# Performance work log

Hardware: AMD Instinct MI355X
Metric: run time of the kernel (lower is better)

Reference implementation:

```python
import jax, jax.numpy as jnp
import numpy as np

PAD = 0
B, M, N, E = 32, 512, 512, 768
NEG_INF = 1e12
SCALE = np.float32(np.sqrt(768.0))


def submult(a, b):
    d = a - b
    return jnp.concatenate([a, b, d, a * b, d * d], axis=-1)


def setup_inputs() -> dict:
    key = jax.random.key(0)
    ks = jax.random.split(key, 8)
    c_ids = jax.random.randint(ks[0], (B, M), 1, 30000)
    c_ids = c_ids.at[:, 3 * M // 4 :].set(PAD)  # trailing padding
    r_ids = jax.random.randint(ks[1], (B, N), 1, 30000)
    r_ids = r_ids.at[:, 3 * N // 4 :].set(PAD)
    c_hs = jax.random.normal(ks[2], (B, M, E), dtype=jnp.float32)
    r_hs = jax.random.normal(ks[3], (B, N, E), dtype=jnp.float32)
    W_pre = jax.random.normal(ks[4], (5 * E, E), dtype=jnp.float32) * 0.02
    b_pre = jnp.zeros((E,), dtype=jnp.float32)
    W_ff1 = jax.random.normal(ks[5], (15 * E, E), dtype=jnp.float32) * 0.02
    b_ff1 = jnp.zeros((E,), dtype=jnp.float32)
    W_ff2 = jax.random.normal(ks[6], (E, 1), dtype=jnp.float32) * 0.02
    b_ff2 = jnp.zeros((1,), dtype=jnp.float32)
    return {
        "c_ids": c_ids, "r_ids": r_ids, "c_hs": c_hs, "r_hs": r_hs,
        "W_pre": W_pre, "b_pre": b_pre,
        "W_ff1": W_ff1, "b_ff1": b_ff1, "W_ff2": W_ff2, "b_ff2": b_ff2,
    }


def reference(c_ids, r_ids, c_hs, r_hs, W_pre, b_pre, W_ff1, b_ff1, W_ff2, b_ff2):
    cm = c_ids != PAD  # [B,M]
    rm = r_ids != PAD  # [B,N]
    # bidirectional cross-attention
    att = jnp.einsum("bme,bne->bmn", c_hs, r_hs) / SCALE
    pair_mask = cm[:, :, None] & rm[:, None, :]
    att = jnp.where(pair_mask, att, -NEG_INF)
    c_hat = jnp.einsum("bne,bmn->bme", r_hs, jax.nn.softmax(att, axis=-1))
    r_hat = jnp.einsum("bme,bmn->bne", c_hs, jax.nn.softmax(att, axis=-2))
    # submult expansion + pre_rnn (Linear + ReLU)
    c_bar = jax.nn.relu(submult(c_hat, c_hs) @ W_pre + b_pre)  # [B,M,E]
    r_bar = jax.nn.relu(submult(r_hat, r_hs) @ W_pre + b_pre)  # [B,N,E]
    # zero out padded positions
    c_x = jnp.where(cm[:, :, None], c_bar, 0.0)
    r_x = jnp.where(rm[:, :, None], r_bar, 0.0)
    c_cnt = cm.sum(-1).astype(c_x.dtype)[:, None]
    r_cnt = rm.sum(-1).astype(r_x.dtype)[:, None]
    c_feat = jnp.concatenate([c_x[:, 0], c_x.sum(1) / c_cnt, c_x.max(1)], axis=-1)
    r_feat = jnp.concatenate([r_x[:, 0], r_x.sum(1) / r_cnt, r_x.max(1)], axis=-1)
    m_vs = submult(c_feat, r_feat)  # [B, 15*E]
    h = jax.nn.relu(m_vs @ W_ff1 + b_ff1)
    scores = (h @ W_ff2 + b_ff2)[:, 0]  # [B]
    return scores
```

## Files before the change

### kernel.cpp

```cpp
#include <hip/hip_runtime.h>
#include <math.h>

#define B_ 32
#define M_ 512
#define N_ 512
#define E_ 768
#define NEG_BIG   -1e12f
#define INV_SCALE 0.03608439182435161f

typedef __attribute__((ext_vector_type(8))) __bf16 bf16x8;
typedef __attribute__((ext_vector_type(4))) float  floatx4;

#define MFMA_BF16 __builtin_amdgcn_mfma_f32_16x16x32_bf16

#define BAR() do { asm volatile("s_waitcnt lgkmcnt(0)" ::: "memory"); \
                   __builtin_amdgcn_s_barrier(); } while (0)

__device__ __forceinline__ void load16(const float* __restrict__ p, float* v) {
    *(float4*)&v[0]  = *(const float4*)(p);
    *(float4*)&v[4]  = *(const float4*)(p + 4);
    *(float4*)&v[8]  = *(const float4*)(p + 8);
    *(float4*)&v[12] = *(const float4*)(p + 12);
}

__device__ __forceinline__ void cvt_store16(const float* v, __bf16* hi, __bf16* lo,
                                            int row, int h) {
    bf16x8 h0, h1, l0, l1;
#pragma unroll
    for (int j = 0; j < 8; ++j) {
        float x0 = v[j], x1 = v[j + 8];
        __bf16 a0 = (__bf16)x0;
        __bf16 a1 = (__bf16)x1;
        h0[j] = a0;
        h1[j] = a1;
        l0[j] = (__bf16)(x0 - (float)a0);
        l1[j] = (__bf16)(x1 - (float)a1);
    }
    const int xr = (row >> 1) & 3;
    *(bf16x8*)&hi[row * 32 + (((2 * h)     ^ xr) << 3)] = h0;
    *(bf16x8*)&hi[row * 32 + (((2 * h + 1) ^ xr) << 3)] = h1;
    *(bf16x8*)&lo[row * 32 + (((2 * h)     ^ xr) << 3)] = l0;
    *(bf16x8*)&lo[row * 32 + (((2 * h + 1) ^ xr) << 3)] = l1;
}

__device__ __forceinline__ void store_pre16(const bf16x8* v, __bf16* hi, __bf16* lo,
                                            int row, int h) {
    const int xr = (row >> 1) & 3;
    *(bf16x8*)&hi[row * 32 + (((2 * h)     ^ xr) << 3)] = v[0];
    *(bf16x8*)&hi[row * 32 + (((2 * h + 1) ^ xr) << 3)] = v[1];
    *(bf16x8*)&lo[row * 32 + (((2 * h)     ^ xr) << 3)] = v[2];
    *(bf16x8*)&lo[row * 32 + (((2 * h + 1) ^ xr) << 3)] = v[3];
}

__device__ __forceinline__ void mfma_step(const __bf16* Ahi, const __bf16* Alo,
                                          const __bf16* Bhi, const __bf16* Blo,
                                          const int (&aoff)[4], const int (&boff)[4],
                                          floatx4 (&acc)[4][4]) {
    bf16x8 bh[4], bl[4];
#pragma unroll
    for (int fn = 0; fn < 4; ++fn) {
        bh[fn] = *(const bf16x8*)&Bhi[boff[fn]];
        bl[fn] = *(const bf16x8*)&Blo[boff[fn]];
    }
#pragma unroll
    for (int fm = 0; fm < 4; ++fm) {
        bf16x8 ah = *(const bf16x8*)&Ahi[aoff[fm]];
        bf16x8 al = *(const bf16x8*)&Alo[aoff[fm]];
#pragma unroll
        for (int fn = 0; fn < 4; ++fn) {
            acc[fm][fn] = MFMA_BF16(ah, bh[fn], acc[fm][fn], 0, 0, 0);
            acc[fm][fn] = MFMA_BF16(ah, bl[fn], acc[fm][fn], 0, 0, 0);
            acc[fm][fn] = MFMA_BF16(al, bh[fn], acc[fm][fn], 0, 0, 0);
        }
    }
}

#define TILE_SETUP()                                                      \
    const int tid = threadIdx.x, lane = tid & 63;                         \
    const int l15 = lane & 15, l4 = lane >> 4;                            \
    const int wid = tid >> 6, wm = wid >> 1, wn = wid & 1;                \
    const int srow = tid >> 1, h = tid & 1;                               \
    int aoff[4], boff[4];                                                 \
    _Pragma("unroll")                                                     \
    for (int f = 0; f < 4; ++f) {                                         \
        int rr = wm * 64 + f * 16 + l15;                                  \
        aoff[f] = rr * 32 + ((l4 ^ ((rr >> 1) & 3)) << 3);                \
        int cc = wn * 64 + f * 16 + l15;                                  \
        boff[f] = cc * 32 + ((l4 ^ ((cc >> 1) & 3)) << 3);                \
    }                                                                     \
    floatx4 acc[4][4];                                                    \
    const floatx4 zero_ = {0.f, 0.f, 0.f, 0.f};                           \
    _Pragma("unroll")                                                     \
    for (int i = 0; i < 4; ++i)                                           \
        _Pragma("unroll")                                                 \
        for (int j = 0; j < 4; ++j) acc[i][j] = zero_;

__global__ __launch_bounds__(256, 2)
void mfma_att(const float* __restrict__ chs, const float* __restrict__ rhs,
              const int* __restrict__ cids, const int* __restrict__ rids,
              float* __restrict__ att) {
    __shared__ __bf16 Ahi[4096], Alo[4096], Bhi[4096], Blo[4096];
    const int b = blockIdx.z, m0 = blockIdx.x * 128, n0 = blockIdx.y * 128;
    TILE_SETUP();
    const float* Ap = chs + ((size_t)b * M_ + m0 + srow) * E_ + h * 16;
    const float* Bp = rhs + ((size_t)b * N_ + n0 + srow) * E_ + h * 16;

    float va[16], vb[16], na[16], nb[16];
    load16(Ap, va); load16(Bp, vb);
#pragma unroll 1
    for (int k0 = 0; k0 < E_; k0 += 64) {
        BAR();
        cvt_store16(va, Ahi, Alo, srow, h);
        cvt_store16(vb, Bhi, Blo, srow, h);
        load16(Ap + k0 + 32, na);
        load16(Bp + k0 + 32, nb);
        BAR();
        mfma_step(Ahi, Alo, Bhi, Blo, aoff, boff, acc);
        BAR();
        cvt_store16(na, Ahi, Alo, srow, h);
        cvt_store16(nb, Bhi, Blo, srow, h);
        if (k0 + 64 < E_) { load16(Ap + k0 + 64, va); load16(Bp + k0 + 64, vb); }
        BAR();
        mfma_step(Ahi, Alo, Bhi, Blo, aoff, boff, acc);
    }

    bool rm[4];
#pragma unroll
    for (int fn = 0; fn < 4; ++fn)
        rm[fn] = rids[b * N_ + n0 + wn * 64 + fn * 16 + l15] != 0;
    float* Cb = att + (size_t)b * M_ * N_;
#pragma unroll
    for (int fm = 0; fm < 4; ++fm) {
        const int rbase = m0 + wm * 64 + fm * 16 + l4 * 4;
#pragma unroll
        for (int r = 0; r < 4; ++r) {
            const int row = rbase + r;
            const bool cm = cids[b * M_ + row] != 0;
#pragma unroll
            for (int fn = 0; fn < 4; ++fn) {
                float vv = (cm && rm[fn]) ? acc[fm][fn][r] * INV_SCALE : NEG_BIG;
                Cb[(size_t)row * N_ + n0 + wn * 64 + fn * 16 + l15] = vv;
            }
        }
    }
}

__global__ __launch_bounds__(256, 2)
void mfma_nn(const __bf16* __restrict__ Phi, const __bf16* __restrict__ Plo,
             const float* __restrict__ Bg, float* __restrict__ C) {
    __shared__ __bf16 Ahi[4096], Alo[4096], Bhi[4096], Blo[4096];
    __shared__ float scr[32 * 132];
    const int b = blockIdx.z, m0 = blockIdx.x * 128, n0 = blockIdx.y * 128;
    TILE_SETUP();
    const __bf16* Aph = Phi + ((size_t)b * 512 + m0 + srow) * 512 + h * 16;
    const __bf16* Apl = Plo + ((size_t)b * 512 + m0 + srow) * 512 + h * 16;
    const int kk = tid >> 3, cseg = (tid & 7) * 16;
    const float* Bp = Bg + ((size_t)b * 512 + kk) * E_ + n0 + cseg;

    bf16x8 a0[4], a1[4];
    float w0[16], w1[16];
    a0[0] = *(const bf16x8*)(Aph);     a0[1] = *(const bf16x8*)(Aph + 8);
    a0[2] = *(const bf16x8*)(Apl);     a0[3] = *(const bf16x8*)(Apl + 8);
    load16(Bp, w0);
#pragma unroll 1
    for (int k0 = 0; k0 < 512; k0 += 64) {
        BAR();
        store_pre16(a0, Ahi, Alo, srow, h);
        *(float4*)&scr[kk * 132 + cseg]      = *(float4*)&w0[0];
        *(float4*)&scr[kk * 132 + cseg + 4]  = *(float4*)&w0[4];
        *(float4*)&scr[kk * 132 + cseg + 8]  = *(float4*)&w0[8];
        *(float4*)&scr[kk * 132 + cseg + 12] = *(float4*)&w0[12];
        a1[0] = *(const bf16x8*)(Aph + k0 + 32);
        a1[1] = *(const bf16x8*)(Aph + k0 + 40);
        a1[2] = *(const bf16x8*)(Apl + k0 + 32);
        a1[3] = *(const bf16x8*)(Apl + k0 + 40);
        load16(Bp + (size_t)(k0 + 32) * E_, w1);
        BAR();
        {
            float vb16[16];
#pragma unroll
            for (int j = 0; j < 16; ++j) vb16[j] = scr[(h * 16 + j) * 132 + srow];
            cvt_store16(vb16, Bhi, Blo, srow, h);
        }
        BAR();
        mfma_step(Ahi, Alo, Bhi, Blo, aoff, boff, acc);
        BAR();
        store_pre16(a1, Ahi, Alo, srow, h);
        *(float4*)&scr[kk * 132 + cseg]      = *(float4*)&w1[0];
        *(float4*)&scr[kk * 132 + cseg + 4]  = *(float4*)&w1[4];
        *(float4*)&scr[kk * 132 + cseg + 8]  = *(float4*)&w1[8];
        *(float4*)&scr[kk * 132 + cseg + 12] = *(float4*)&w1[12];
        if (k0 + 64 < 512) {
            a0[0] = *(const bf16x8*)(Aph + k0 + 64);
            a0[1] = *(const bf16x8*)(Aph + k0 + 72);
            a0[2] = *(const bf16x8*)(Apl + k0 + 64);
            a0[3] = *(const bf16x8*)(Apl + k0 + 72);
            load16(Bp + (size_t)(k0 + 64) * E_, w0);
        }
        BAR();
        {
            float vb16[16];
#pragma unroll
            for (int j = 0; j < 16; ++j) vb16[j] = scr[(h * 16 + j) * 132 + srow];
            cvt_store16(vb16, Bhi, Blo, srow, h);
        }
        BAR();
        mfma_step(Ahi, Alo, Bhi, Blo, aoff, boff, acc);
    }

    float* Cb = C + (size_t)b * M_ * E_;
#pragma unroll
    for (int fm = 0; fm < 4; ++fm) {
        const int rbase = m0 + wm * 64 + fm * 16 + l4 * 4;
#pragma unroll
        for (int r = 0; r < 4; ++r)
#pragma unroll
            for (int fn = 0; fn < 4; ++fn)
                Cb[(size_t)(rbase + r) * E_ + n0 + wn * 64 + fn * 16 + l15] =
                    acc[fm][fn][r];
    }
}

__device__ __forceinline__ void feature16(float* f, const float* a, const float* s,
                                          int seg) {
    if (seg == 0) {
#pragma unroll
        for (int j = 0; j < 16; ++j) f[j] = a[j];
    } else if (seg == 1) {
#pragma unroll
        for (int j = 0; j < 16; ++j) f[j] = s[j];
    } else if (seg == 2) {
#pragma unroll
        for (int j = 0; j < 16; ++j) f[j] = a[j] - s[j];
    } else if (seg == 3) {
#pragma unroll
        for (int j = 0; j < 16; ++j) f[j] = a[j] * s[j];
    } else {
#pragma unroll
        for (int j = 0; j < 16; ++j) { float d = a[j] - s[j]; f[j] = d * d; }
    }
}

__global__ __launch_bounds__(256, 2)
void mfma_feat(const float* __restrict__ chat, const float* __restrict__ rhat,
               const float* __restrict__ chs, const float* __restrict__ rhs,
               const __bf16* __restrict__ WThi, const __bf16* __restrict__ WTlo,
               const float* __restrict__ bias, const int* __restrict__ cids,
               const int* __restrict__ rids, float* __restrict__ scs,
               float* __restrict__ srs) {
    __shared__ __bf16 Ahi[4096], Alo[4096], Bhi[4096], Blo[4096];
    const int side = blockIdx.z;
    const float* HAT = side ? rhat : chat;
    const float* HS  = side ? rhs  : chs;
    const int*   ids = side ? rids : cids;
    float*     stats = side ? srs  : scs;
    const int m0 = blockIdx.x * 128, n0 = blockIdx.y * 128;
    TILE_SETUP();
    const float* Hp = HAT + (size_t)(m0 + srow) * E_ + h * 16;
    const float* Sp = HS  + (size_t)(m0 + srow) * E_ + h * 16;
    const __bf16* Wph = WThi + (size_t)(n0 + srow) * 3840 + h * 16;
    const __bf16* Wpl = WTlo + (size_t)(n0 + srow) * 3840 + h * 16;

    float a0v[16], s0v[16], a1v[16], s1v[16];
    bf16x8 w0[4], w1[4];
    load16(Hp, a0v); load16(Sp, s0v);
    w0[0] = *(const bf16x8*)(Wph);     w0[1] = *(const bf16x8*)(Wph + 8);
    w0[2] = *(const bf16x8*)(Wpl);     w0[3] = *(const bf16x8*)(Wpl + 8);

#pragma unroll 1
    for (int t = 0; t < 120; t += 2) {
        {
            float f[16];
            feature16(f, a0v, s0v, t / 24);
            BAR();
            cvt_store16(f, Ahi, Alo, srow, h);
            store_pre16(w0, Bhi, Blo, srow, h);
            const int t1 = t + 1;
            const int e1 = (t1 % 24) * 32;
            load16(Hp + e1, a1v); load16(Sp + e1, s1v);
            w1[0] = *(const bf16x8*)(Wph + t1 * 32);
            w1[1] = *(const bf16x8*)(Wph + t1 * 32 + 8);
            w1[2] = *(const bf16x8*)(Wpl + t1 * 32);
            w1[3] = *(const bf16x8*)(Wpl + t1 * 32 + 8);
            BAR();
            mfma_step(Ahi, Alo, Bhi, Blo, aoff, boff, acc);
        }
        {
            float f[16];
            feature16(f, a1v, s1v, (t + 1) / 24);
            BAR();
            cvt_store16(f, Ahi, Alo, srow, h);
            store_pre16(w1, Bhi, Blo, srow, h);
            if (t + 2 < 120) {
                const int t2 = t + 2;
                const int e2 = (t2 % 24) * 32;
                load16(Hp + e2, a0v); load16(Sp + e2, s0v);
                w0[0] = *(const bf16x8*)(Wph + t2 * 32);
                w0[1] = *(const bf16x8*)(Wph + t2 * 32 + 8);
                w0[2] = *(const bf16x8*)(Wpl + t2 * 32);
                w0[3] = *(const bf16x8*)(Wpl + t2 * 32 + 8);
            }
            BAR();
            mfma_step(Ahi, Alo, Bhi, Blo, aoff, boff, acc);
        }
    }

    const int b = m0 >> 9;
    float bv[4];
#pragma unroll
    for (int fn = 0; fn < 4; ++fn)
        bv[fn] = bias[n0 + wn * 64 + fn * 16 + l15];
    float sum4[4] = {0.f, 0.f, 0.f, 0.f}, max4[4] = {0.f, 0.f, 0.f, 0.f};
#pragma unroll
    for (int fm = 0; fm < 4; ++fm) {
        const int rbase = m0 + wm * 64 + fm * 16 + l4 * 4;
#pragma unroll
        for (int r = 0; r < 4; ++r) {
            const int g = rbase + r;
            const bool valid = ids[g] != 0;
#pragma unroll
            for (int fn = 0; fn < 4; ++fn) {
                float v = fmaxf(acc[fm][fn][r] + bv[fn], 0.f);
                v = valid ? v : 0.f;
                sum4[fn] += v;
                max4[fn] = fmaxf(max4[fn], v);
                if ((g & 511) == 0)
                    stats[b * 2304 + n0 + wn * 64 + fn * 16 + l15] = v;
            }
        }
    }
#pragma unroll
    for (int fn = 0; fn < 4; ++fn) {
        float s = sum4[fn];
        s += __shfl_xor(s, 16); s += __shfl_xor(s, 32);
        float mx = max4[fn];
        mx = fmaxf(mx, __shfl_xor(mx, 16)); mx = fmaxf(mx, __shfl_xor(mx, 32));
        if (l4 == 0) {
            const int col = n0 + wn * 64 + fn * 16 + l15;
            atomicAdd(&stats[b * 2304 + 768 + col], s);
            atomicMax((int*)&stats[b * 2304 + 1536 + col], __float_as_int(mx));
        }
    }
}

__global__ __launch_bounds__(256)
void split_w(const float* __restrict__ src, __bf16* __restrict__ whi,
             __bf16* __restrict__ wlo) {
    __shared__ float tile[32][33];
    const int c0 = blockIdx.x * 32;
    const int r0 = blockIdx.y * 32;
    const int tx = threadIdx.x & 31, ty = threadIdx.x >> 5;
#pragma unroll
    for (int i = 0; i < 32; i += 8)
        tile[ty + i][tx] = src[(size_t)(r0 + ty + i) * 768 + c0 + tx];
    __syncthreads();
    const int nr = threadIdx.x >> 3, kq = (threadIdx.x & 7) * 4;
#pragma unroll
    for (int j = 0; j < 4; ++j) {
        float v = tile[kq + j][nr];
        __bf16 hv = (__bf16)v;
        whi[(size_t)(c0 + nr) * 3840 + r0 + kq + j] = hv;
        wlo[(size_t)(c0 + nr) * 3840 + r0 + kq + j] = (__bf16)(v - (float)hv);
    }
}

__global__ __launch_bounds__(256)
void softmax_rows(const float* __restrict__ att, __bf16* __restrict__ phi,
                  __bf16* __restrict__ plo) {
    const int wave = threadIdx.x >> 6;
    const int lane = threadIdx.x & 63;
    const size_t row = (size_t)blockIdx.x * 4 + wave;
    const float* x = att + row * N_;
    float v[8];
    float mx = -INFINITY;
#pragma unroll
    for (int i = 0; i < 8; ++i) { v[i] = x[lane + i * 64]; mx = fmaxf(mx, v[i]); }
#pragma unroll
    for (int off = 32; off; off >>= 1) mx = fmaxf(mx, __shfl_xor(mx, off));
    float s = 0.f;
#pragma unroll
    for (int i = 0; i < 8; ++i) { v[i] = __expf(v[i] - mx); s += v[i]; }
#pragma unroll
    for (int off = 32; off; off >>= 1) s += __shfl_xor(s, off);
    const float inv = 1.f / s;
#pragma unroll
    for (int i = 0; i < 8; ++i) {
        float val = v[i] * inv;
        __bf16 hv = (__bf16)val;
        phi[row * N_ + lane + i * 64] = hv;
        plo[row * N_ + lane + i * 64] = (__bf16)(val - (float)hv);
    }
}

__global__ __launch_bounds__(256)
void softmax_cols_t(const float* __restrict__ att, __bf16* __restrict__ dhi,
                    __bf16* __restrict__ dlo) {
    __shared__ float tile[512][17];
    __shared__ float red[16][16];
    __shared__ float invs[16];
    const int b = blockIdx.x, n0 = blockIdx.y * 16;
    const int tid = threadIdx.x;
    const int c = tid & 15, r = tid >> 4;
    const float* src = att + (size_t)b * M_ * N_ + n0;
#pragma unroll 4
    for (int i = 0; i < 32; ++i) {
        int m = r + i * 16;
        tile[m][c] = src[(size_t)m * N_ + c];
    }
    __syncthreads();
    float mx = -INFINITY;
    for (int m = r; m < 512; m += 16) mx = fmaxf(mx, tile[m][c]);
    red[r][c] = mx;
    __syncthreads();
    if (r == 0) {
        float m2 = red[0][c];
#pragma unroll
        for (int j = 1; j < 16; ++j) m2 = fmaxf(m2, red[j][c]);
        invs[c] = m2;
    }
    __syncthreads();
    const float cmx = invs[c];
    float s = 0.f;
    for (int m = r; m < 512; m += 16) {
        float e = __expf(tile[m][c] - cmx);
        tile[m][c] = e;
        s += e;
    }
    __syncthreads();
    red[r][c] = s;
    __syncthreads();
    if (r == 0) {
        float st = 0.f;
#pragma unroll
        for (int j = 0; j < 16; ++j) st += red[j][c];
        invs[c] = 1.f / st;
    }
    __syncthreads();
#pragma unroll 4
    for (int i = 0; i < 32; ++i) {
        int lin = tid + i * 256;
        int cc = lin >> 9;
        int m = lin & 511;
        float val = tile[m][cc] * invs[cc];
        __bf16 hv = (__bf16)val;
        const size_t o = ((size_t)b * N_ + n0 + cc) * M_ + m;
        dhi[o] = hv;
        dlo[o] = (__bf16)(val - (float)hv);
    }
}

__global__ __launch_bounds__(256)
void ffprep_kernel(const float* __restrict__ sc, const float* __restrict__ sr,
                   const int* __restrict__ cids, const int* __restrict__ rids,
                   float* __restrict__ mv) {
    __shared__ int redc[4], redr[4];
    const int b = blockIdx.x, tid = threadIdx.x;
    int cc = 0, cr = 0;
    for (int m = tid; m < 512; m += 256) {
        cc += (cids[b * 512 + m] != 0);
        cr += (rids[b * 512 + m] != 0);
    }
#pragma unroll
    for (int off = 32; off; off >>= 1) {
        cc += __shfl_xor(cc, off);
        cr += __shfl_xor(cr, off);
    }
    if ((tid & 63) == 0) { redc[tid >> 6] = cc; redr[tid >> 6] = cr; }
    __syncthreads();
    const float invc = 1.f / (float)(redc[0] + redc[1] + redc[2] + redc[3]);
    const float invr = 1.f / (float)(redr[0] + redr[1] + redr[2] + redr[3]);
    const float* scb = sc + b * 2304;
    const float* srb = sr + b * 2304;
    float* mvb = mv + (size_t)b * 11520;
    for (int i = tid; i < 2304; i += 256) {
        float a = scb[i], r = srb[i];
        if (i >= 768 && i < 1536) { a *= invc; r *= invr; }
        float d = a - r;
        mvb[i]        = a;
        mvb[2304 + i] = r;
        mvb[4608 + i] = d;
        mvb[6912 + i] = a * r;
        mvb[9216 + i] = d * d;
    }
}

__global__ __launch_bounds__(256)
void ff1_kernel(const float* __restrict__ mv, const float* __restrict__ W1,
                float* __restrict__ hacc) {
    const int j = blockIdx.x * 256 + threadIdx.x;
    const int e0 = blockIdx.y * 720;
    float acc[32];
#pragma unroll
    for (int b = 0; b < 32; ++b) acc[b] = 0.f;
    for (int ec = 0; ec < 720; ec += 4) {
        const float w0 = W1[(size_t)(e0 + ec + 0) * 768 + j];
        const float w1 = W1[(size_t)(e0 + ec + 1) * 768 + j];
        const float w2 = W1[(size_t)(e0 + ec + 2) * 768 + j];
        const float w3 = W1[(size_t)(e0 + ec + 3) * 768 + j];
#pragma unroll
        for (int b = 0; b < 32; ++b) {
            const float* mp = mv + (size_t)b * 11520 + e0 + ec;
            float a = acc[b];
            a = fmaf(mp[0], w0, a);
            a = fmaf(mp[1], w1, a);
            a = fmaf(mp[2], w2, a);
            a = fmaf(mp[3], w3, a);
            acc[b] = a;
        }
    }
#pragma unroll
    for (int b = 0; b < 32; ++b) atomicAdd(&hacc[b * 768 + j], acc[b]);
}

__global__ __launch_bounds__(256)
void score_kernel(const float* __restrict__ hacc, const float* __restrict__ b1,
                  const float* __restrict__ W2, const float* __restrict__ b2,
                  float* __restrict__ out) {
    const int b = blockIdx.x, tid = threadIdx.x;
    float acc = 0.f;
    for (int j = tid; j < 768; j += 256)
        acc += fmaxf(hacc[b * 768 + j] + b1[j], 0.f) * W2[j];
#pragma unroll
    for (int off = 32; off; off >>= 1) acc += __shfl_xor(acc, off);
    __shared__ float red[4];
    if ((tid & 63) == 0) red[tid >> 6] = acc;
    __syncthreads();
    if (tid == 0) out[b] = red[0] + red[1] + red[2] + red[3] + b2[0];
}

extern "C" void kernel_launch(void* const* d_in, const int* in_sizes, int n_in,
                              void* d_out, int out_size, void* d_ws, size_t ws_size,
                              hipStream_t stream) {
    const int*   c_ids = (const int*)d_in[0];
    const int*   r_ids = (const int*)d_in[1];
    const float* c_hs  = (const float*)d_in[2];
    const float* r_hs  = (const float*)d_in[3];
    const float* W_pre = (const float*)d_in[4];
    const float* b_pre = (const float*)d_in[5];
    const float* W_ff1 = (const float*)d_in[6];
    const float* b_ff1 = (const float*)d_in[7];
    const float* W_ff2 = (const float*)d_in[8];
    const float* b_ff2 = (const float*)d_in[9];
    float* out = (float*)d_out;
    float* ws  = (float*)d_ws;

    float* att   = ws;
    __bf16* P1hi  = (__bf16*)(ws + 8388608);
    __bf16* P1lo  = (__bf16*)(ws + 12582912);
    __bf16* P2thi = (__bf16*)(ws + 16777216);
    __bf16* P2tlo = (__bf16*)(ws + 20971520);
    float* chat  = ws + 25165824;
    float* rhat  = ws;
    __bf16* WThi  = (__bf16*)(ws + 12582912);
    __bf16* WTlo  = (__bf16*)(ws + 14057472);
    float* sc    = ws + 15532032;
    float* sr    = sc + 73728;
    float* hacc  = sr + 73728;
    float* mv    = hacc + 24576;

    mfma_att<<<dim3(4, 4, 32), 256, 0, stream>>>(c_hs, r_hs, c_ids, r_ids, att);
    softmax_rows  <<<dim3(B_ * M_ / 4), 256, 0, stream>>>(att, P1hi, P1lo);
    softmax_cols_t<<<dim3(B_, 32), 256, 0, stream>>>(att, P2thi, P2tlo);
    mfma_nn<<<dim3(4, 6, 32), 256, 0, stream>>>(P1hi, P1lo, r_hs, chat);
    split_w<<<dim3(24, 120), 256, 0, stream>>>(W_pre, WThi, WTlo);
    hipMemsetAsync(sc, 0, 172032 * sizeof(float), stream);
    mfma_nn<<<dim3(4, 6, 32), 256, 0, stream>>>(P2thi, P2tlo, c_hs, rhat);
    mfma_feat<<<dim3(128, 6, 2), 256, 0, stream>>>(chat, rhat, c_hs, r_hs,
                                                   WThi, WTlo, b_pre,
                                                   c_ids, r_ids, sc, sr);
    ffprep_kernel<<<dim3(32), 256, 0, stream>>>(sc, sr, c_ids, r_ids, mv);
    ff1_kernel<<<dim3(3, 16), 256, 0, stream>>>(mv, W_ff1, hacc);
    score_kernel<<<dim3(32), 256, 0, stream>>>(hacc, b_ff1, W_ff2, b_ff2, out);
}
```

Before: 1.519 ms.

## Fold submult difference segment into combined W_pre, shrinking feature GEMM K

Uses the identity [a,b,a-b,ab,(a-b)^2]·W = a·(W0+W2) + b·(W1-W2) + ab·W3 + (a-b)^2·W4, so W_pre is folded into a 4E×E weight during the split kernel. This cuts the feature GEMM reduction from 3840 to 3072 and removes one feature segment. The single z=2 launch is split into two separate launches, one for the context side and one for the response side. Folding the weights changes rounding slightly before the bf16 hi/lo split.

Result: faster. 1.443 ms (-5.0%).

```diff
diff --git a/kernel.cpp b/kernel.cpp
--- a/kernel.cpp
+++ b/kernel.cpp
@@ -231,9 +231,6 @@
         for (int j = 0; j < 16; ++j) f[j] = s[j];
     } else if (seg == 2) {
 #pragma unroll
-        for (int j = 0; j < 16; ++j) f[j] = a[j] - s[j];
-    } else if (seg == 3) {
-#pragma unroll
         for (int j = 0; j < 16; ++j) f[j] = a[j] * s[j];
     } else {
 #pragma unroll
@@ -242,24 +239,17 @@
 }
 
 __global__ __launch_bounds__(256, 2)
-void mfma_feat(const float* __restrict__ chat, const float* __restrict__ rhat,
-               const float* __restrict__ chs, const float* __restrict__ rhs,
+void mfma_feat(const float* __restrict__ HAT, const float* __restrict__ HS,
                const __bf16* __restrict__ WThi, const __bf16* __restrict__ WTlo,
-               const float* __restrict__ bias, const int* __restrict__ cids,
-               const int* __restrict__ rids, float* __restrict__ scs,
-               float* __restrict__ srs) {
+               const float* __restrict__ bias, const int* __restrict__ ids,
+               float* __restrict__ stats) {
     __shared__ __bf16 Ahi[4096], Alo[4096], Bhi[4096], Blo[4096];
-    const int side = blockIdx.z;
-    const float* HAT = side ? rhat : chat;
-    const float* HS  = side ? rhs  : chs;
-    const int*   ids = side ? rids : cids;
-    float*     stats = side ? srs  : scs;
     const int m0 = blockIdx.x * 128, n0 = blockIdx.y * 128;
     TILE_SETUP();
     const float* Hp = HAT + (size_t)(m0 + srow) * E_ + h * 16;
     const float* Sp = HS  + (size_t)(m0 + srow) * E_ + h * 16;
-    const __bf16* Wph = WThi + (size_t)(n0 + srow) * 3840 + h * 16;
-    const __bf16* Wpl = WTlo + (size_t)(n0 + srow) * 3840 + h * 16;
+    const __bf16* Wph = WThi + (size_t)(n0 + srow) * 3072 + h * 16;
+    const __bf16* Wpl = WTlo + (size_t)(n0 + srow) * 3072 + h * 16;
 
     float a0v[16], s0v[16], a1v[16], s1v[16];
     bf16x8 w0[4], w1[4];
@@ -268,7 +258,7 @@
     w0[2] = *(const bf16x8*)(Wpl);     w0[3] = *(const bf16x8*)(Wpl + 8);
 
 #pragma unroll 1
-    for (int t = 0; t < 120; t += 2) {
+    for (int t = 0; t < 96; t += 2) {
         {
             float f[16];
             feature16(f, a0v, s0v, t / 24);
@@ -291,7 +281,7 @@
             BAR();
             cvt_store16(f, Ahi, Alo, srow, h);
             store_pre16(w1, Bhi, Blo, srow, h);
-            if (t + 2 < 120) {
+            if (t + 2 < 96) {
                 const int t2 = t + 2;
                 const int e2 = (t2 % 24) * 32;
                 load16(Hp + e2, a0v); load16(Sp + e2, s0v);
@@ -344,23 +334,35 @@
 }
 
 __global__ __launch_bounds__(256)
-void split_w(const float* __restrict__ src, __bf16* __restrict__ whi,
-             __bf16* __restrict__ wlo) {
+void combine_w(const float* __restrict__ src, __bf16* __restrict__ whi,
+               __bf16* __restrict__ wlo) {
     __shared__ float tile[32][33];
     const int c0 = blockIdx.x * 32;
     const int r0 = blockIdx.y * 32;
+    const int seg = r0 / 768, e0 = r0 % 768;
     const int tx = threadIdx.x & 31, ty = threadIdx.x >> 5;
 #pragma unroll
-    for (int i = 0; i < 32; i += 8)
-        tile[ty + i][tx] = src[(size_t)(r0 + ty + i) * 768 + c0 + tx];
+    for (int i = 0; i < 32; i += 8) {
+        const int e = e0 + ty + i;
+        float v;
+        if (seg == 0)
+            v = src[(size_t)e * 768 + c0 + tx] + src[(size_t)(1536 + e) * 768 + c0 + tx];
+        else if (seg == 1)
+            v = src[(size_t)(768 + e) * 768 + c0 + tx] - src[(size_t)(1536 + e) * 768 + c0 + tx];
+        else if (seg == 2)
+            v = src[(size_t)(2304 + e) * 768 + c0 + tx];
+        else
+            v = src[(size_t)(3072 + e) * 768 + c0 + tx];
+        tile[ty + i][tx] = v;
+    }
     __syncthreads();
     const int nr = threadIdx.x >> 3, kq = (threadIdx.x & 7) * 4;
 #pragma unroll
     for (int j = 0; j < 4; ++j) {
         float v = tile[kq + j][nr];
         __bf16 hv = (__bf16)v;
-        whi[(size_t)(c0 + nr) * 3840 + r0 + kq + j] = hv;
-        wlo[(size_t)(c0 + nr) * 3840 + r0 + kq + j] = (__bf16)(v - (float)hv);
+        whi[(size_t)(c0 + nr) * 3072 + r0 + kq + j] = hv;
+        wlo[(size_t)(c0 + nr) * 3072 + r0 + kq + j] = (__bf16)(v - (float)hv);
     }
 }
 
@@ -552,7 +554,7 @@
     float* chat  = ws + 25165824;
     float* rhat  = ws;
     __bf16* WThi  = (__bf16*)(ws + 12582912);
-    __bf16* WTlo  = (__bf16*)(ws + 14057472);
+    __bf16* WTlo  = (__bf16*)(ws + 13762560);
     float* sc    = ws + 15532032;
     float* sr    = sc + 73728;
     float* hacc  = sr + 73728;
@@ -562,12 +564,13 @@
     softmax_rows  <<<dim3(B_ * M_ / 4), 256, 0, stream>>>(att, P1hi, P1lo);
     softmax_cols_t<<<dim3(B_, 32), 256, 0, stream>>>(att, P2thi, P2tlo);
     mfma_nn<<<dim3(4, 6, 32), 256, 0, stream>>>(P1hi, P1lo, r_hs, chat);
-    split_w<<<dim3(24, 120), 256, 0, stream>>>(W_pre, WThi, WTlo);
+    combine_w<<<dim3(24, 96), 256, 0, stream>>>(W_pre, WThi, WTlo);
     hipMemsetAsync(sc, 0, 172032 * sizeof(float), stream);
     mfma_nn<<<dim3(4, 6, 32), 256, 0, stream>>>(P2thi, P2tlo, c_hs, rhat);
-    mfma_feat<<<dim3(128, 6, 2), 256, 0, stream>>>(chat, rhat, c_hs, r_hs,
-                                                   WThi, WTlo, b_pre,
-                                                   c_ids, r_ids, sc, sr);
+    mfma_feat<<<dim3(128, 6), 256, 0, stream>>>(chat, c_hs, WThi, WTlo, b_pre,
+                                                c_ids, sc);
+    mfma_feat<<<dim3(128, 6), 256, 0, stream>>>(rhat, r_hs, WThi, WTlo, b_pre,
+                                                r_ids, sr);
     ffprep_kernel<<<dim3(32), 256, 0, stream>>>(sc, sr, c_ids, r_ids, mv);
     ff1_kernel<<<dim3(3, 16), 256, 0, stream>>>(mv, W_ff1, hacc);
     score_kernel<<<dim3(32), 256, 0, stream>>>(hacc, b_ff1, W_ff2, b_ff2, out);
```
